# Kernel tuning notes

Hardware: AMD Instinct MI355X
Metric: run time of the kernel (lower is better)

The kernel has to match this reference:

```python
import jax, jax.numpy as jnp
import numpy as np

# Hyperparameters matching init_kwargs
IN_CH = 64
OUT_CH = 128
KERNEL = (3, 3)
STRIDE = (1, 1)
PADDING = 'SAME'
K_ORDER = 3          # spline order
G_INTERVALS = 3      # grid intervals
GRID_MIN, GRID_MAX = -1.0, 1.0
N_BASIS = G_INTERVALS + K_ORDER  # basis functions per input = 6
PATCH_DIM = IN_CH * KERNEL[0] * KERNEL[1]  # 576


def _grid():
    # Extended uniform knot vector: G + 2k + 1 knots
    h = (GRID_MAX - GRID_MIN) / G_INTERVALS
    return jnp.arange(-K_ORDER, G_INTERVALS + K_ORDER + 1, dtype=jnp.float32) * h + GRID_MIN


def _b_splines(x):
    # x: [N, n_in] -> bases: [N, n_in, G + k]
    grid = _grid()  # [G + 2k + 1]
    xe = x[..., None]  # [N, n_in, 1]
    bases = ((xe >= grid[:-1]) & (xe < grid[1:])).astype(x.dtype)  # order-0, [N, n_in, G+2k]
    for p in range(1, K_ORDER + 1):
        left = (xe - grid[: -(p + 1)]) / (grid[p:-1] - grid[: -(p + 1)]) * bases[..., :-1]
        right = (grid[p + 1:] - xe) / (grid[p + 1:] - grid[1:-p]) * bases[..., 1:]
        bases = left + right
    return bases  # [N, n_in, G + k]


def setup_inputs() -> dict:
    key = jax.random.key(0)
    k0, k1, k2, k3 = jax.random.split(key, 4)
    x = jax.random.normal(k0, (8, 64, 64, IN_CH), dtype=jnp.float32)
    base_w = jax.random.normal(k1, (OUT_CH, PATCH_DIM), dtype=jnp.float32) * 0.05
    spline_w = jax.random.normal(k2, (OUT_CH, PATCH_DIM, N_BASIS), dtype=jnp.float32) * 0.05
    bias = jax.random.normal(k3, (OUT_CH,), dtype=jnp.float32) * 0.05
    return {'x': x, 'base_w': base_w, 'spline_w': spline_w, 'bias': bias}


def reference(x, base_w, spline_w, bias):
    batch = x.shape[0]
    dn = ('NHWC', 'HWIO', 'NHWC')
    patches = jax.lax.conv_general_dilated_patches(
        lhs=x, filter_shape=KERNEL, window_strides=STRIDE, padding=PADDING,
        dimension_numbers=dn)  # [B, H, W, patch_dim]
    out_spatial = patches.shape[1:-1]
    p = patches.reshape(-1, PATCH_DIM)  # [N, patch_dim]
    # EfficientKAN: residual (silu) branch + spline branch + bias
    base_out = jax.nn.silu(p) @ base_w.T                      # [N, out]
    bases = _b_splines(p)                                      # [N, patch_dim, G+k]
    spline_out = jnp.einsum('nig,oig->no', bases, spline_w)    # [N, out]
    y = base_out + spline_out + bias
    return y.reshape(batch, *out_spatial, OUT_CH)
```

## Files before the change

### kernel.cpp

```cpp
#include <hip/hip_runtime.h>

typedef __attribute__((ext_vector_type(8))) short short8;
typedef __attribute__((ext_vector_type(16))) float f32x16;

#define FT2_SHORTS (512u * 4356u * 8u)
#define PLANE16    4356

typedef __attribute__((address_space(3))) unsigned int lds_u32_t;
typedef __attribute__((address_space(1))) const unsigned int g_u32_t;

__device__ __forceinline__ unsigned short f2bf(float x) {
    union { float f; unsigned u; } v; v.f = x;
    unsigned r = v.u + 0x7FFFu + ((v.u >> 16) & 1u);
    return (unsigned short)(r >> 16);
}

__device__ __forceinline__ void feat8(float p, unsigned short* uf) {
    float e   = __expf(-p);
    float sig = 1.f / (1.f + e);
    uf[0] = f2bf(p * sig);
    float u  = p * 1.5f + 4.5f;
    float fj = floorf(u);
    int   j0 = (int)fj;
    float t  = u - fj;
    bool  inr = (u >= 0.f) && (u < 9.f);
    float t2 = t * t, t3 = t2 * t;
    const float c16 = 1.f / 6.f;
    float r0 = t3 * c16;
    float r1 = (-3.f * t3 + 3.f * t2 + 3.f * t + 1.f) * c16;
    float r2 = (3.f * t3 - 6.f * t2 + 4.f) * c16;
    float s1 = 1.f - t;
    float r3 = s1 * s1 * s1 * c16;
#pragma unroll
    for (int g = 0; g < 6; ++g) {
        int r = j0 - g;
        float v = (r == 0) ? r0 : ((r == 1) ? r1 : ((r == 2) ? r2 : ((r == 3) ? r3 : 0.f)));
        uf[1 + g] = f2bf(inr ? v : 0.f);
    }
    uf[7] = 0;
}

__global__ __launch_bounds__(256)
void prep_all(const float* __restrict__ x,
              const float* __restrict__ bw, const float* __restrict__ sw,
              unsigned short* __restrict__ ft, unsigned short* __restrict__ wt) {
    const int blk = blockIdx.x;
    const int tid = threadIdx.x;

    if (tid < 144) {
        int idx = blk * 144 + tid;
        int o = idx / 576;
        int i = idx - o * 576;
        int slab = i >> 3, e = i & 7;
        union { unsigned short u[8]; uint4 v; } pk;
        pk.u[0] = f2bf(bw[o * 576 + i]);
        const float* s = sw + (size_t)(o * 576 + i) * 6;
#pragma unroll
        for (int f = 0; f < 6; ++f) pk.u[1 + f] = f2bf(s[f]);
        pk.u[7] = 0;
        *(uint4*)(wt + ((size_t)slab * 8192 + e * 1024 + o * 8)) = pk.v;
    }

    {
        short8 pad = { 0, 0, (short)0x3CAB, (short)0x3EF5,
                       (short)0x3EF5, (short)0x3CAB, 0, 0 };
        for (int t = tid; t < 260; t += 256) {
            int yy, xx;
            if (t < 66)       { yy = 0;       xx = t; }
            else if (t < 132) { yy = 65;      xx = t - 66; }
            else if (t < 196) { yy = t - 131; xx = 0; }
            else              { yy = t - 195; xx = 65; }
            ((short8*)ft)[blk * PLANE16 + yy * 66 + xx] = pad;
        }
    }

    __shared__ float Xl[64 * 65];
    const int b = blk >> 6, y = blk & 63;
    const float* xl = x + (size_t)blk * 4096;
    for (int f4 = tid; f4 < 1024; f4 += 256) {
        float4 v = ((const float4*)xl)[f4];
        int xx = f4 >> 4, c4 = (f4 & 15) << 2;
        float* d = &Xl[xx * 65 + c4];
        d[0] = v.x; d[1] = v.y; d[2] = v.z; d[3] = v.w;
    }
    __syncthreads();
    const int xx = tid & 63;
    const int cw = tid >> 6;
#pragma unroll 4
    for (int p = 0; p < 16; ++p) {
        int c = cw + (p << 2);
        float pv = Xl[xx * 65 + c];
        union { unsigned short u[8]; uint4 v; } pk;
        feat8(pv, pk.u);
        size_t o16 = (size_t)(c * 8 + b) * PLANE16 + (y + 1) * 66 + (xx + 1);
        *(uint4*)(ft + (o16 << 3)) = pk.v;
    }
}

#define BUF_SHORTS 24576

#define STAGE(sl, q_)                                                                 \
    {                                                                                 \
        unsigned short* bufq = Bufs + (q_) * BUF_SHORTS;                              \
        const unsigned short* bsrc = wt + (size_t)(slab0 + (sl)) * 8192;              \
        _Pragma("unroll")                                                             \
        for (int r = 0; r < 2; ++r) {                                                 \
            int boff = (r * 8 + wave) * 512 + lane * 8;                               \
            __builtin_amdgcn_global_load_lds((g_u32_t*)(bsrc + boff),                 \
                                             (lds_u32_t*)(bufq + boff), 16, 0, 0);    \
        }                                                                             \
        _Pragma("unroll")                                                             \
        for (int t = 0; t < 4; ++t) {                                                 \
            int idx = wave * 4 + t;                         \
            int ia  = (slab0 + (sl)) * 8 + (idx >> 2);                                \
            int g2  = idx & 3;                                                        \
            int c_  = (ia * 7282) >> 16;                                              \
            int i9_ = ia - c_ * 9;                                                    \
            int kh_ = (i9_ * 11) >> 5;                                                \
            int kw_ = i9_ - kh_ * 3;                                                  \
            const unsigned short* asrc = ft +                                         \
                (((size_t)(c_ * 8 + b) * PLANE16 + (y0 + g2 + kh_) * 66 + kw_) << 3)  \
                + lane * 8;                                                           \
            unsigned short* adst = bufq + 8192 + idx * 512 + lane * 8;                \
            __builtin_amdgcn_global_load_lds((g_u32_t*)asrc, (lds_u32_t*)adst,        \
                                             16, 0, 0);                               \
        }                                                                             \
    }

#define KSTEP(s_)                                                                     \
    {                                                                                 \
        int iloc = 2 * (s_) + h;                                                      \
        const unsigned short* Ab = bufr + 8192 + (iloc * 4 + g) * 512;                \
        const unsigned short* Bb = bufr + iloc * 1024;                                \
        short8 a0 = *(const short8*)(Ab + l32 * 8);                                   \
        short8 a1 = *(const short8*)(Ab + (32 + l32) * 8);                            \
        short8 b0 = *(const short8*)(Bb + (nh * 64 + l32) * 8);                       \
        short8 b1 = *(const short8*)(Bb + (nh * 64 + 32 + l32) * 8);                  \
        acc00 = __builtin_amdgcn_mfma_f32_32x32x16_bf16(a0, b0, acc00, 0, 0, 0);      \
        acc01 = __builtin_amdgcn_mfma_f32_32x32x16_bf16(a0, b1, acc01, 0, 0, 0);      \
        acc10 = __builtin_amdgcn_mfma_f32_32x32x16_bf16(a1, b0, acc10, 0, 0, 0);      \
        acc11 = __builtin_amdgcn_mfma_f32_32x32x16_bf16(a1, b1, acc11, 0, 0, 0);      \
    }

#define PHASE(it_, q_, n_, dostage_)                                                  \
    {                                                                                 \
        asm volatile("s_waitcnt vmcnt(" #n_ ")" ::: "memory");                        \
        __builtin_amdgcn_s_barrier();                                                 \
        asm volatile("" ::: "memory");                                                \
        const unsigned short* bufr = Bufs + (q_) * BUF_SHORTS;                        \
        __builtin_amdgcn_s_setprio(1);                                                \
        KSTEP(0) KSTEP(1) KSTEP(2) KSTEP(3)                                           \
        __builtin_amdgcn_s_setprio(0);                                                \
        asm volatile("" ::: "memory");                                                \
        __builtin_amdgcn_s_barrier();                                                 \
        asm volatile("" ::: "memory");                                                \
        if (dostage_) STAGE((it_) + 3, q_);                                           \
    }

__global__ __launch_bounds__(512, 2)
void convkan_gemm(const unsigned short* __restrict__ ft,
                  const unsigned short* __restrict__ wt,
                  const float* __restrict__ bias,
                  float* __restrict__ out) {
    extern __shared__ unsigned short Bufs[];

    const int tid  = threadIdx.x;
    const int blk  = blockIdx.x;
    const int kk   = blk & 1;
    const int mb   = blk >> 1;
    const int lane = tid & 63;
    const int wave = tid >> 6;
    const int g    = wave >> 1;
    const int nh   = wave & 1;
    const int l32  = lane & 31;
    const int h    = lane >> 5;

    const int b  = mb >> 4;
    const int y0 = (mb & 15) << 2;
    const int slab0 = kk * 36;

    f32x16 acc00, acc01, acc10, acc11;
#pragma unroll
    for (int e = 0; e < 16; ++e) { acc00[e] = 0.f; acc01[e] = 0.f; acc10[e] = 0.f; acc11[e] = 0.f; }

    STAGE(0, 0);
    STAGE(1, 1);
    STAGE(2, 2);

    for (int it3 = 0; it3 < 11; ++it3) {
        const int it = it3 * 3;
        PHASE(it + 0, 0, 12, true)
        PHASE(it + 1, 1, 12, true)
        PHASE(it + 2, 2, 12, true)
    }
    PHASE(33, 0, 12, false)
    PHASE(34, 1, 6,  false)
    PHASE(35, 2, 0,  false)

    const float bv0 = kk ? 0.f : bias[nh * 64 + l32];
    const float bv1 = kk ? 0.f : bias[nh * 64 + 32 + l32];
    const int prow = (mb * 4 + g) * 64;
    const int ncol = nh * 64 + l32;
#pragma unroll
    for (int r = 0; r < 16; ++r) {
        int mrow = (r & 3) + ((r >> 2) << 3) + 4 * h;
        float* p0 = out + (size_t)(prow + mrow) * 128 + ncol;
        float* p1 = out + (size_t)(prow + 32 + mrow) * 128 + ncol;
        atomicAdd(p0,      acc00[r] + bv0);
        atomicAdd(p0 + 32, acc01[r] + bv1);
        atomicAdd(p1,      acc10[r] + bv0);
        atomicAdd(p1 + 32, acc11[r] + bv1);
    }
}

extern "C" void kernel_launch(void* const* d_in, const int* in_sizes, int n_in,
                              void* d_out, int out_size, void* d_ws, size_t ws_size,
                              hipStream_t stream) {
    (void)in_sizes; (void)n_in; (void)ws_size;
    const float* x        = (const float*)d_in[0];
    const float* base_w   = (const float*)d_in[1];
    const float* spline_w = (const float*)d_in[2];
    const float* bias     = (const float*)d_in[3];
    float* out = (float*)d_out;

    unsigned short* ft = (unsigned short*)d_ws;
    unsigned short* wt = ft + FT2_SHORTS;

    hipMemsetAsync(out, 0, (size_t)out_size * sizeof(float), stream);
    hipLaunchKernelGGL(prep_all, dim3(512), dim3(256), 0, stream,
                       x, base_w, spline_w, ft, wt);

    const int shmem = 3 * BUF_SHORTS * 2;
    (void)hipFuncSetAttribute((const void*)convkan_gemm,
                              hipFuncAttributeMaxDynamicSharedMemorySize, shmem);
    hipLaunchKernelGGL(convkan_gemm, dim3(256), dim3(512), shmem, stream,
                       ft, wt, bias, out);
}
```

Before: 146.8 us.

## Drop split-K atomics; use 128-row tiles with full K per block

Each GEMM block now covers 2 output rows (128 pixels) and runs the full K range over 72 slabs, instead of splitting K in two and combining partials with atomicAdd. Output is written with plain stores and the bias is added directly, which removes the memset and the atomic traffic. Each wave now holds two accumulators instead of four, and the LDS stage per buffer shrinks. In exchange, each block loops twice as long and each wave does half as much MFMA work per staged slab, so data reuse per load is lower.

```diff
diff --git a/kernel.cpp b/kernel.cpp
--- a/kernel.cpp
+++ b/kernel.cpp
@@ -97,49 +97,47 @@
     }
 }
 
-#define BUF_SHORTS 24576
+#define BUF_SHORTS 16384
 
 #define STAGE(sl, q_)                                                                 \
     {                                                                                 \
         unsigned short* bufq = Bufs + (q_) * BUF_SHORTS;                              \
-        const unsigned short* bsrc = wt + (size_t)(slab0 + (sl)) * 8192;              \
-        _Pragma("unroll")                                                             \
-        for (int r = 0; r < 2; ++r) {                                                 \
-            int boff = (r * 8 + wave) * 512 + lane * 8;                               \
-            __builtin_amdgcn_global_load_lds((g_u32_t*)(bsrc + boff),                 \
-                                             (lds_u32_t*)(bufq + boff), 16, 0, 0);    \
-        }                                                                             \
+        const unsigned short* bsrc = wt + (size_t)(sl) * 8192;                        \
         _Pragma("unroll")                                                             \
         for (int t = 0; t < 4; ++t) {                                                 \
-            int idx = wave * 4 + t;                         \
-            int ia  = (slab0 + (sl)) * 8 + (idx >> 2);                                \
-            int g2  = idx & 3;                                                        \
-            int c_  = (ia * 7282) >> 16;                                              \
-            int i9_ = ia - c_ * 9;                                                    \
-            int kh_ = (i9_ * 11) >> 5;                                                \
-            int kw_ = i9_ - kh_ * 3;                                                  \
-            const unsigned short* asrc = ft +                                         \
-                (((size_t)(c_ * 8 + b) * PLANE16 + (y0 + g2 + kh_) * 66 + kw_) << 3)  \
-                + lane * 8;                                                           \
-            unsigned short* adst = bufq + 8192 + idx * 512 + lane * 8;                \
-            __builtin_amdgcn_global_load_lds((g_u32_t*)asrc, (lds_u32_t*)adst,        \
-                                             16, 0, 0);                               \
+            int u = wave * 4 + t;                     \
+            if (u < 16) {                                                             \
+                int boff = u * 512 + lane * 8;                                        \
+                __builtin_amdgcn_global_load_lds((g_u32_t*)(bsrc + boff),             \
+                                                 (lds_u32_t*)(bufq + boff), 16, 0, 0);\
+            } else {                                                                  \
+                int ua  = u - 16;                                     \
+                int ia  = (sl) * 8 + (ua >> 1);                                       \
+                int ln  = ua & 1;                                                     \
+                int c_  = (ia * 7282) >> 16;                                          \
+                int i9_ = ia - c_ * 9;                                                \
+                int kh_ = (i9_ * 11) >> 5;                                            \
+                int kw_ = i9_ - kh_ * 3;                                              \
+                const unsigned short* asrc = ft +                                     \
+                    (((size_t)(c_ * 8 + b) * PLANE16 + (y0 + ln + kh_) * 66 + kw_)    \
+                     << 3) + lane * 8;                                                \
+                unsigned short* adst = bufq + 8192 + ua * 512 + lane * 8;             \
+                __builtin_amdgcn_global_load_lds((g_u32_t*)asrc, (lds_u32_t*)adst,    \
+                                                 16, 0, 0);                           \
+            }                                                                         \
         }                                                                             \
     }
 
 #define KSTEP(s_)                                                                     \
     {                                                                                 \
-        int iloc = 2 * (s_) + h;                                                      \
-        const unsigned short* Ab = bufr + 8192 + (iloc * 4 + g) * 512;                \
+        int iloc = 2 * (s_) + h;                                    \
+        const unsigned short* Ab = bufr + 8192 + ((iloc << 1) + gl) * 512;            \
         const unsigned short* Bb = bufr + iloc * 1024;                                \
-        short8 a0 = *(const short8*)(Ab + l32 * 8);                                   \
-        short8 a1 = *(const short8*)(Ab + (32 + l32) * 8);                            \
+        short8 a0 = *(const short8*)(Ab + (gh * 32 + l32) * 8);                       \
         short8 b0 = *(const short8*)(Bb + (nh * 64 + l32) * 8);                       \
         short8 b1 = *(const short8*)(Bb + (nh * 64 + 32 + l32) * 8);                  \
-        acc00 = __builtin_amdgcn_mfma_f32_32x32x16_bf16(a0, b0, acc00, 0, 0, 0);      \
-        acc01 = __builtin_amdgcn_mfma_f32_32x32x16_bf16(a0, b1, acc01, 0, 0, 0);      \
-        acc10 = __builtin_amdgcn_mfma_f32_32x32x16_bf16(a1, b0, acc10, 0, 0, 0);      \
-        acc11 = __builtin_amdgcn_mfma_f32_32x32x16_bf16(a1, b1, acc11, 0, 0, 0);      \
+        acc0 = __builtin_amdgcn_mfma_f32_32x32x16_bf16(a0, b0, acc0, 0, 0, 0);        \
+        acc1 = __builtin_amdgcn_mfma_f32_32x32x16_bf16(a0, b1, acc1, 0, 0, 0);        \
     }
 
 #define PHASE(it_, q_, n_, dostage_)                                                  \
@@ -165,58 +163,54 @@
     extern __shared__ unsigned short Bufs[];
 
     const int tid  = threadIdx.x;
-    const int blk  = blockIdx.x;
-    const int kk   = blk & 1;
-    const int mb   = blk >> 1;
+    const int mb   = blockIdx.x;
     const int lane = tid & 63;
     const int wave = tid >> 6;
     const int g    = wave >> 1;
     const int nh   = wave & 1;
+    const int gl   = g >> 1;
+    const int gh   = g & 1;
     const int l32  = lane & 31;
     const int h    = lane >> 5;
 
-    const int b  = mb >> 4;
-    const int y0 = (mb & 15) << 2;
-    const int slab0 = kk * 36;
-
-    f32x16 acc00, acc01, acc10, acc11;
-#pragma unroll
-    for (int e = 0; e < 16; ++e) { acc00[e] = 0.f; acc01[e] = 0.f; acc10[e] = 0.f; acc11[e] = 0.f; }
+    const int b  = mb >> 5;
+    const int y0 = (mb & 31) << 1;
+
+    f32x16 acc0, acc1;
+#pragma unroll
+    for (int e = 0; e < 16; ++e) { acc0[e] = 0.f; acc1[e] = 0.f; }
 
     STAGE(0, 0);
     STAGE(1, 1);
     STAGE(2, 2);
 
-    for (int it3 = 0; it3 < 11; ++it3) {
+    for (int it3 = 0; it3 < 23; ++it3) {
         const int it = it3 * 3;
-        PHASE(it + 0, 0, 12, true)
-        PHASE(it + 1, 1, 12, true)
-        PHASE(it + 2, 2, 12, true)
-    }
-    PHASE(33, 0, 12, false)
-    PHASE(34, 1, 6,  false)
-    PHASE(35, 2, 0,  false)
-
-    const float bv0 = kk ? 0.f : bias[nh * 64 + l32];
-    const float bv1 = kk ? 0.f : bias[nh * 64 + 32 + l32];
-    const int prow = (mb * 4 + g) * 64;
+        PHASE(it + 0, 0, 8, true)
+        PHASE(it + 1, 1, 8, true)
+        PHASE(it + 2, 2, 8, true)
+    }
+    PHASE(69, 0, 8, false)
+    PHASE(70, 1, 4, false)
+    PHASE(71, 2, 0, false)
+
     const int ncol = nh * 64 + l32;
+    const float bv0 = bias[ncol];
+    const float bv1 = bias[ncol + 32];
+    const int prow = mb * 128 + g * 32;
 #pragma unroll
     for (int r = 0; r < 16; ++r) {
         int mrow = (r & 3) + ((r >> 2) << 3) + 4 * h;
-        float* p0 = out + (size_t)(prow + mrow) * 128 + ncol;
-        float* p1 = out + (size_t)(prow + 32 + mrow) * 128 + ncol;
-        atomicAdd(p0,      acc00[r] + bv0);
-        atomicAdd(p0 + 32, acc01[r] + bv1);
-        atomicAdd(p1,      acc10[r] + bv0);
-        atomicAdd(p1 + 32, acc11[r] + bv1);
+        float* p = out + (size_t)(prow + mrow) * 128 + ncol;
+        p[0]  = acc0[r] + bv0;
+        p[32] = acc1[r] + bv1;
     }
 }
 
 extern "C" void kernel_launch(void* const* d_in, const int* in_sizes, int n_in,
                               void* d_out, int out_size, void* d_ws, size_t ws_size,
                               hipStream_t stream) {
-    (void)in_sizes; (void)n_in; (void)ws_size;
+    (void)in_sizes; (void)n_in; (void)ws_size; (void)out_size;
     const float* x        = (const float*)d_in[0];
     const float* base_w   = (const float*)d_in[1];
     const float* spline_w = (const float*)d_in[2];
@@ -226,7 +220,6 @@
     unsigned short* ft = (unsigned short*)d_ws;
     unsigned short* wt = ft + FT2_SHORTS;
 
-    hipMemsetAsync(out, 0, (size_t)out_size * sizeof(float), stream);
     hipLaunchKernelGGL(prep_all, dim3(512), dim3(256), 0, stream,
                        x, base_w, spline_w, ft, wt);
 
```

Measured after the change: 140.7 us. 1.04x faster.
